# Kernel optimization log

Measured on AMD Instinct MI355X. Metric: run time of the kernel, lower is better.

The kernel has to match this reference:

```python
import jax, jax.numpy as jnp
import numpy as np


def position_encoding(feature_size, d_model):
    pos = jnp.arange(feature_size, dtype=jnp.float32)[:, None]
    _2i = jnp.arange(0, d_model, 2, dtype=jnp.float32)
    ang = pos / jnp.power(10000.0, _2i / d_model)  # [F, D/2]
    pe = jnp.zeros((feature_size, d_model), dtype=jnp.float32)
    pe = pe.at[:, 0::2].set(jnp.sin(ang))
    pe = pe.at[:, 1::2].set(jnp.cos(ang))
    return pe


def setup_inputs() -> dict:
    key = jax.random.key(0)
    ks = jax.random.split(key, 11)
    B, F, D, T, V = 32, 512, 256, 32, 128
    sc = 0.02
    return {
        "f": jax.random.normal(ks[0], (B, F, D), dtype=jnp.float32),
        "decoder_input_ids": jax.random.randint(ks[1], (B, T), 0, V),
        "emb": sc * jax.random.normal(ks[2], (V, D), dtype=jnp.float32),
        "w_e": sc * jax.random.normal(ks[3], (D, D), dtype=jnp.float32),
        "w_h": sc * jax.random.normal(ks[4], (D, D), dtype=jnp.float32),
        "w_f": sc * jax.random.normal(ks[5], (D, D), dtype=jnp.float32),
        "w_q": sc * jax.random.normal(ks[6], (D, D), dtype=jnp.float32),
        "w_s": sc * jax.random.normal(ks[7], (D, D), dtype=jnp.float32),
        "w_g": sc * jax.random.normal(ks[8], (D, 2 * D), dtype=jnp.float32),
        "w_ih": sc * jax.random.normal(ks[9], (4 * D, 2 * D), dtype=jnp.float32),
        "w_hh": sc * jax.random.normal(ks[10], (4 * D, D), dtype=jnp.float32),
    }


def reference(f, decoder_input_ids, emb, w_e, w_h, w_f, w_q, w_s, w_g, w_ih, w_hh):
    B, F, D = f.shape
    q = position_encoding(F, D)                      # [F, D]
    dec = emb[decoder_input_ids]                     # [B, T, D]
    # loop-invariant attention terms, hoisted: w_f(f) + w_q(q)
    base = jnp.einsum('bfd,od->bfo', f, w_f) + (q @ w_q.T)[None]  # [B, F, D]
    fq = f + q[None]                                 # [B, F, D]

    def step(carry, x_t):
        h, cell, s, cp = carry
        # LSTMCell (bias=False), torch gate order i, f, g, o
        xin = jnp.concatenate([x_t, cp], axis=-1)    # [B, 2D]
        gates = xin @ w_ih.T + h @ w_hh.T            # [B, 4D]
        gi, gf, gg, go = jnp.split(gates, 4, axis=-1)
        cell = jax.nn.sigmoid(gf) * cell + jax.nn.sigmoid(gi) * jnp.tanh(gg)
        h = jax.nn.sigmoid(go) * jnp.tanh(cell)
        # Bahdanau-style energy; softmax over feature (last) dim per source
        t_in = jnp.tanh((h @ w_h.T)[:, None] + base + jnp.einsum('bfd,od->bfo', s, w_s))
        e = jnp.einsum('bfd,od->bfo', t_in, w_e)     # [B, F, D]
        alpha = jax.nn.softmax(e, axis=-1)
        s = s + alpha
        c = (alpha * f).sum(1)                       # [B, D]
        cp = (alpha * fq).sum(1)                     # [B, D]
        pred = jnp.concatenate([c, h], axis=-1) @ w_g.T  # [B, D]
        return (h, cell, s, cp), pred

    z = jnp.zeros((B, D), dtype=f.dtype)
    carry0 = (z, z, jnp.zeros_like(f), z)
    _, preds = jax.lax.scan(step, carry0, jnp.swapaxes(dec, 0, 1))  # [T, B, D]
    return jnp.swapaxes(preds, 0, 1)                 # [B, T, D]
```

## Files before the change

kernel.cpp:

```cpp
#include <hip/hip_runtime.h>
#include <math.h>

#define NB 32
#define NF 512
#define ND 256
#define NT 32
#define RPB 32
#define NTILE (NF / RPB)

typedef __attribute__((ext_vector_type(8))) short bf16x8;
typedef __attribute__((ext_vector_type(4))) float f32x4;

__device__ __forceinline__ float sigmoidf_(float x) { return 1.0f / (1.0f + __expf(-x)); }

__device__ __forceinline__ short f2bf(float x) {
    union { float f; unsigned u; } v; v.f = x;
    unsigned r = (v.u + 0x7FFF + ((v.u >> 16) & 1)) >> 16;
    return (short)r;
}

__global__ void pe_kernel(float* __restrict__ q) {
    int p = blockIdx.x;
    int d = threadIdx.x;
    float i2 = (float)((d >> 1) << 1);
    float rate = expf(-9.210340371976184f * (i2 / (float)ND));
    float ang = (float)p * rate;
    q[p * ND + d] = (d & 1) ? cosf(ang) : sinf(ang);
}

__global__ void gather_kernel(const int* __restrict__ ids, const float* __restrict__ emb,
                              float* __restrict__ dec) {
    int bt = blockIdx.x;
    int d = threadIdx.x;
    dec[(size_t)bt * ND + d] = emb[(size_t)ids[bt] * ND + d];
}

__global__ void wcvt_kernel(const float* __restrict__ w, short* __restrict__ wb, int n) {
    int i = blockIdx.x * 256 + threadIdx.x;
    if (i < n) wb[i] = f2bf(w[i]);
}

__global__ void qwq_kernel(const float* __restrict__ q, const float* __restrict__ w_q,
                           float* __restrict__ qwq) {
    int p = blockIdx.x;
    int o = threadIdx.x;
    __shared__ float qs[ND];
    qs[o] = q[(size_t)p * ND + o];
    __syncthreads();
    const float4* wr = (const float4*)(w_q + (size_t)o * ND);
    float acc = 0.f;
    for (int k4 = 0; k4 < ND / 4; ++k4) {
        float4 w = wr[k4];
        int k = 4 * k4;
        acc += qs[k] * w.x + qs[k + 1] * w.y + qs[k + 2] * w.z + qs[k + 3] * w.w;
    }
    qwq[(size_t)p * ND + o] = acc;
}

__global__ void base_kernel(const float* __restrict__ fin, const float* __restrict__ w_f,
                            const float* __restrict__ qwq, float* __restrict__ bsum) {
    int b = blockIdx.x / NTILE;
    int f0 = (blockIdx.x % NTILE) * RPB;
    int o = threadIdx.x;
    __shared__ float fs[RPB][ND];
    #pragma unroll
    for (int r = 0; r < RPB; ++r)
        fs[r][o] = fin[((size_t)(b * NF + f0 + r)) * ND + o];
    __syncthreads();
    float acc[RPB];
    #pragma unroll
    for (int r = 0; r < RPB; ++r) acc[r] = 0.f;
    const float4* wr = (const float4*)(w_f + (size_t)o * ND);
    for (int k4 = 0; k4 < ND / 4; ++k4) {
        float4 w = wr[k4];
        int k = 4 * k4;
        #pragma unroll
        for (int r = 0; r < RPB; ++r)
            acc[r] += fs[r][k] * w.x + fs[r][k + 1] * w.y + fs[r][k + 2] * w.z + fs[r][k + 3] * w.w;
    }
    #pragma unroll
    for (int r = 0; r < RPB; ++r)
        bsum[((size_t)(b * NF + f0 + r)) * ND + o] = acc[r] + qwq[(size_t)(f0 + r) * ND + o];
}

#define ZSTRIDE 769
#define ZPSTRIDE 513
__global__ void gates_kernel(int t, int mode,
                             const float* __restrict__ dec,
                             const float* __restrict__ cpart, const float* __restrict__ cppart,
                             const float* __restrict__ h,
                             const float* __restrict__ w_ih, const float* __restrict__ w_hh,
                             const float* __restrict__ w_g,
                             float* __restrict__ gatesT, float* __restrict__ out) {
    extern __shared__ float lds[];
    int bid = blockIdx.x;
    int tid = threadIdx.x;

    if (bid < 128) {
        if (!(mode & 1)) return;
        int j0 = bid * 8;
        float* wl = lds;
        float* zl = lds + 8 * 768;
        float4* wl4 = (float4*)wl;
        for (int cc = 0; cc < 6; ++cc) {
            int idx4 = tid + cc * 256;
            int flat = idx4 * 4;
            int r = flat / 768;
            int col = flat - r * 768;
            float4 v;
            if (col < 512) v = *(const float4*)(w_ih + (size_t)(j0 + r) * 512 + col);
            else           v = *(const float4*)(w_hh + (size_t)(j0 + r) * 256 + (col - 512));
            wl4[idx4] = v;
        }
        for (int b = 0; b < NB; ++b) {
            int d = tid;
            float xv = (t < NT) ? dec[((size_t)b * NT + t) * ND + d] : 0.f;
            float cpsum = 0.f;
            if (t > 0) {
                #pragma unroll
                for (int tl = 0; tl < NTILE; ++tl)
                    cpsum += cppart[((size_t)tl * NB + b) * ND + d];
            }
            float hv = h[(size_t)b * ND + d];
            zl[b * ZSTRIDE + d]       = xv;
            zl[b * ZSTRIDE + 256 + d] = cpsum;
            zl[b * ZSTRIDE + 512 + d] = hv;
        }
        __syncthreads();
        int r = tid >> 5;
        int b = tid & 31;
        const float4* wr4 = (const float4*)(wl + r * 768);
        const float* zb = zl + b * ZSTRIDE;
        float acc = 0.f;
        #pragma unroll 8
        for (int k4 = 0; k4 < 192; ++k4) {
            float4 w = wr4[k4];
            int k = 4 * k4;
            acc += w.x * zb[k] + w.y * zb[k + 1] + w.z * zb[k + 2] + w.w * zb[k + 3];
        }
        gatesT[(size_t)(j0 + r) * NB + b] = acc;
    } else {
        if (!(mode & 2)) return;
        int p0 = (bid - 128) * 8;
        float* wl = lds;
        float* zl = lds + 8 * 512;
        float4* wl4 = (float4*)wl;
        for (int cc = 0; cc < 4; ++cc) {
            int idx4 = tid + cc * 256;
            int flat = idx4 * 4;
            int r = flat >> 9;
            int col = flat & 511;
            wl4[idx4] = *(const float4*)(w_g + (size_t)(p0 + r) * 512 + col);
        }
        for (int b = 0; b < NB; ++b) {
            float csum = 0.f;
            #pragma unroll
            for (int tl = 0; tl < NTILE; ++tl)
                csum += cpart[((size_t)tl * NB + b) * ND + tid];
            zl[b * ZPSTRIDE + tid]       = csum;
            zl[b * ZPSTRIDE + 256 + tid] = h[(size_t)b * ND + tid];
        }
        __syncthreads();
        int r = tid >> 5;
        int b = tid & 31;
        const float4* wr4 = (const float4*)(wl + r * 512);
        const float* zb = zl + b * ZPSTRIDE;
        float acc = 0.f;
        #pragma unroll 8
        for (int k4 = 0; k4 < 128; ++k4) {
            float4 w = wr4[k4];
            int k = 4 * k4;
            acc += w.x * zb[k] + w.y * zb[k + 1] + w.z * zb[k + 2] + w.w * zb[k + 3];
        }
        out[((size_t)b * NT + (t - 1)) * ND + p0 + r] = acc;
    }
}

__global__ void cell_hwh_kernel(const float* __restrict__ gatesT,
                                float* __restrict__ h, float* __restrict__ cell,
                                const float* __restrict__ w_h, float* __restrict__ hwh) {
    int b = blockIdx.x;
    int o = threadIdx.x;
    __shared__ float hn[ND];
    float gi = gatesT[(size_t)(0 * ND + o) * NB + b];
    float gf = gatesT[(size_t)(1 * ND + o) * NB + b];
    float gg = gatesT[(size_t)(2 * ND + o) * NB + b];
    float go = gatesT[(size_t)(3 * ND + o) * NB + b];
    float cold = cell[(size_t)b * ND + o];
    float cnew = sigmoidf_(gf) * cold + sigmoidf_(gi) * tanhf(gg);
    float hval = sigmoidf_(go) * tanhf(cnew);
    cell[(size_t)b * ND + o] = cnew;
    h[(size_t)b * ND + o] = hval;
    hn[o] = hval;
    __syncthreads();
    const float4* whr = (const float4*)(w_h + (size_t)o * ND);
    float a = 0.f;
    for (int k4 = 0; k4 < ND / 4; ++k4) {
        float4 w = whr[k4]; int k = 4 * k4;
        a += hn[k] * w.x + hn[k + 1] * w.y + hn[k + 2] * w.z + hn[k + 3] * w.w;
    }
    hwh[(size_t)b * ND + o] = a;
}

__global__ void attn_step_kernel(float* __restrict__ bsum,
                                 const float* __restrict__ fin, const float* __restrict__ q,
                                 const float* __restrict__ hwh,
                                 const short* __restrict__ w_e_bf, const short* __restrict__ w_s_bf,
                                 float* __restrict__ cpart, float* __restrict__ cppart) {
    int b = blockIdx.x / NTILE;
    int tile = blockIdx.x % NTILE;
    int f0 = tile * RPB;
    int tid = threadIdx.x;
    int l = tid & 63;
    int wv = tid >> 6;

    __shared__ __align__(16) short tin_bf[RPB * ND];
    __shared__ float sred[RPB][5];

    int o0 = wv * 64;
    int c15 = l & 15;
    int g = l >> 4;
    int kgrp = g * 8;
    char* tb = (char*)tin_bf;

    float bsv[2][4][4];
    {
        float hv4[4];
        #pragma unroll
        for (int nt = 0; nt < 4; ++nt)
            hv4[nt] = hwh[(size_t)b * ND + o0 + nt * 16 + c15];
        #pragma unroll
        for (int mt = 0; mt < 2; ++mt)
            #pragma unroll
            for (int reg = 0; reg < 4; ++reg) {
                int r = mt * 16 + g * 4 + reg;
                size_t rowb = ((size_t)(b * NF + f0 + r)) * ND;
                #pragma unroll
                for (int nt = 0; nt < 4; ++nt) {
                    int col = o0 + nt * 16 + c15;
                    float bs = bsum[rowb + col];
                    bsv[mt][nt][reg] = bs;
                    float tv = tanhf(hv4[nt] + bs);
                    int byte = (r * 512 + col * 2) ^ ((r & 7) << 4);
                    *(short*)(tb + byte) = f2bf(tv);
                }
            }
    }
    __syncthreads();

    f32x4 acc[2][4];
    #pragma unroll
    for (int mt = 0; mt < 2; ++mt)
        #pragma unroll
        for (int nt = 0; nt < 4; ++nt)
            acc[mt][nt] = (f32x4)0.f;
    #pragma unroll
    for (int ks = 0; ks < 8; ++ks) {
        int kb = ks * 32 + kgrp;
        bf16x8 afr[2];
        #pragma unroll
        for (int mt = 0; mt < 2; ++mt) {
            int row = mt * 16 + c15;
            int byte = (row * 512 + kb * 2) ^ ((row & 7) << 4);
            afr[mt] = *(const bf16x8*)(tb + byte);
        }
        #pragma unroll
        for (int nt = 0; nt < 4; ++nt) {
            int o = o0 + nt * 16 + c15;
            bf16x8 bfr = *(const bf16x8*)(w_e_bf + (size_t)o * ND + kb);
            #pragma unroll
            for (int mt = 0; mt < 2; ++mt)
                acc[mt][nt] = __builtin_amdgcn_mfma_f32_16x16x32_bf16(afr[mt], bfr, acc[mt][nt], 0, 0, 0);
        }
    }

    float ps[2][4];
    #pragma unroll
    for (int mt = 0; mt < 2; ++mt)
        #pragma unroll
        for (int reg = 0; reg < 4; ++reg) ps[mt][reg] = 0.f;
    #pragma unroll
    for (int mt = 0; mt < 2; ++mt)
        #pragma unroll
        for (int nt = 0; nt < 4; ++nt)
            #pragma unroll
            for (int reg = 0; reg < 4; ++reg) {
                float a = __expf(acc[mt][nt][reg]);
                acc[mt][nt][reg] = a;
                ps[mt][reg] += a;
            }
    #pragma unroll
    for (int off = 1; off <= 8; off <<= 1)
        #pragma unroll
        for (int mt = 0; mt < 2; ++mt)
            #pragma unroll
            for (int reg = 0; reg < 4; ++reg)
                ps[mt][reg] += __shfl_xor(ps[mt][reg], off);
    if (c15 == 0) {
        #pragma unroll
        for (int mt = 0; mt < 2; ++mt)
            #pragma unroll
            for (int reg = 0; reg < 4; ++reg)
                sred[mt * 16 + g * 4 + reg][wv] = ps[mt][reg];
    }
    __syncthreads();
    float inv[2][4];
    #pragma unroll
    for (int mt = 0; mt < 2; ++mt)
        #pragma unroll
        for (int reg = 0; reg < 4; ++reg) {
            int r = mt * 16 + g * 4 + reg;
            inv[mt][reg] = 1.0f / (sred[r][0] + sred[r][1] + sred[r][2] + sred[r][3]);
        }
    #pragma unroll
    for (int mt = 0; mt < 2; ++mt)
        #pragma unroll
        for (int nt = 0; nt < 4; ++nt)
            #pragma unroll
            for (int reg = 0; reg < 4; ++reg)
                acc[mt][nt][reg] *= inv[mt][reg];

    {
        float pc[4], pcp[4];
        #pragma unroll
        for (int nt = 0; nt < 4; ++nt) { pc[nt] = 0.f; pcp[nt] = 0.f; }
        #pragma unroll
        for (int mt = 0; mt < 2; ++mt)
            #pragma unroll
            for (int reg = 0; reg < 4; ++reg) {
                int r = mt * 16 + g * 4 + reg;
                size_t rowb = ((size_t)(b * NF + f0 + r)) * ND;
                size_t qrowb = (size_t)(f0 + r) * ND;
                #pragma unroll
                for (int nt = 0; nt < 4; ++nt) {
                    int col = o0 + nt * 16 + c15;
                    float a = acc[mt][nt][reg];
                    float fv = fin[rowb + col];
                    float qv = q[qrowb + col];
                    pc[nt] += a * fv;
                    pcp[nt] += a * (fv + qv);
                }
            }
        #pragma unroll
        for (int off = 16; off <= 32; off <<= 1)
            #pragma unroll
            for (int nt = 0; nt < 4; ++nt) {
                pc[nt]  += __shfl_xor(pc[nt], off);
                pcp[nt] += __shfl_xor(pcp[nt], off);
            }
        if (g == 0) {
            #pragma unroll
            for (int nt = 0; nt < 4; ++nt) {
                int col = o0 + nt * 16 + c15;
                cpart [((size_t)tile * NB + b) * ND + col] = pc[nt];
                cppart[((size_t)tile * NB + b) * ND + col] = pcp[nt];
            }
        }
    }

    #pragma unroll
    for (int mt = 0; mt < 2; ++mt)
        #pragma unroll
        for (int reg = 0; reg < 4; ++reg) {
            int r = mt * 16 + g * 4 + reg;
            #pragma unroll
            for (int nt = 0; nt < 4; ++nt) {
                int col = o0 + nt * 16 + c15;
                int byte = (r * 512 + col * 2) ^ ((r & 7) << 4);
                *(short*)(tb + byte) = f2bf(acc[mt][nt][reg]);
            }
        }
    __syncthreads();

    {
        f32x4 acc2[2][4];
        #pragma unroll
        for (int mt = 0; mt < 2; ++mt)
            #pragma unroll
            for (int nt = 0; nt < 4; ++nt)
                acc2[mt][nt] = (f32x4)0.f;
        #pragma unroll
        for (int ks = 0; ks < 8; ++ks) {
            int kb = ks * 32 + kgrp;
            bf16x8 afr[2];
            #pragma unroll
            for (int mt = 0; mt < 2; ++mt) {
                int row = mt * 16 + c15;
                int byte = (row * 512 + kb * 2) ^ ((row & 7) << 4);
                afr[mt] = *(const bf16x8*)(tb + byte);
            }
            #pragma unroll
            for (int nt = 0; nt < 4; ++nt) {
                int o = o0 + nt * 16 + c15;
                bf16x8 bfr = *(const bf16x8*)(w_s_bf + (size_t)o * ND + kb);
                #pragma unroll
                for (int mt = 0; mt < 2; ++mt)
                    acc2[mt][nt] = __builtin_amdgcn_mfma_f32_16x16x32_bf16(afr[mt], bfr, acc2[mt][nt], 0, 0, 0);
            }
        }
        #pragma unroll
        for (int mt = 0; mt < 2; ++mt)
            #pragma unroll
            for (int reg = 0; reg < 4; ++reg) {
                int r = mt * 16 + g * 4 + reg;
                size_t rowb = ((size_t)(b * NF + f0 + r)) * ND;
                #pragma unroll
                for (int nt = 0; nt < 4; ++nt) {
                    int col = o0 + nt * 16 + c15;
                    bsum[rowb + col] = bsv[mt][nt][reg] + acc2[mt][nt][reg];
                }
            }
    }
}

extern "C" void kernel_launch(void* const* d_in, const int* in_sizes, int n_in,
                              void* d_out, int out_size, void* d_ws, size_t ws_size,
                              hipStream_t stream) {
    const float* fin  = (const float*)d_in[0];
    const int*   ids  = (const int*)  d_in[1];
    const float* emb  = (const float*)d_in[2];
    const float* w_e  = (const float*)d_in[3];
    const float* w_h  = (const float*)d_in[4];
    const float* w_f  = (const float*)d_in[5];
    const float* w_q  = (const float*)d_in[6];
    const float* w_s  = (const float*)d_in[7];
    const float* w_g  = (const float*)d_in[8];
    const float* w_ih = (const float*)d_in[9];
    const float* w_hh = (const float*)d_in[10];
    float* out = (float*)d_out;
    float* ws  = (float*)d_ws;

    size_t off = 0;
    float* q      = ws + off; off += (size_t)NF * ND;
    float* scratch= ws + off; off += (size_t)NF * ND;
    float* dec    = ws + off; off += (size_t)NB * NT * ND;
    float* bsum   = ws + off; off += (size_t)NB * NF * ND;
    float* h      = ws + off; off += (size_t)NB * ND;
    float* cell   = ws + off; off += (size_t)NB * ND;
    float* hwh    = ws + off; off += (size_t)NB * ND;
    float* cpart  = ws + off; off += (size_t)NTILE * NB * ND;
    float* cppart = ws + off; off += (size_t)NTILE * NB * ND;
    short* w_e_bf = (short*)(ws + off); off += (size_t)ND * ND / 2;
    short* w_s_bf = (short*)(ws + off); off += (size_t)ND * ND / 2;

    float* qwq    = scratch;
    float* gatesT = scratch + 65536;

    hipMemsetAsync(h, 0, sizeof(float) * NB * ND, stream);
    hipMemsetAsync(cell, 0, sizeof(float) * NB * ND, stream);

    pe_kernel<<<NF, ND, 0, stream>>>(q);
    gather_kernel<<<NB * NT, ND, 0, stream>>>(ids, emb, dec);
    wcvt_kernel<<<ND * ND / 256, 256, 0, stream>>>(w_e, w_e_bf, ND * ND);
    wcvt_kernel<<<ND * ND / 256, 256, 0, stream>>>(w_s, w_s_bf, ND * ND);
    qwq_kernel<<<NF, ND, 0, stream>>>(q, w_q, qwq);
    base_kernel<<<NB * NTILE, ND, 0, stream>>>(fin, w_f, qwq, bsum);

    const size_t gates_lds = (size_t)(8 * 768 + NB * ZSTRIDE) * sizeof(float);

    for (int t = 0; t < NT; ++t) {
        int mode = (t > 0) ? 3 : 1;
        gates_kernel<<<160, ND, gates_lds, stream>>>(t, mode, dec, cpart, cppart, h,
                                                     w_ih, w_hh, w_g, gatesT, out);
        cell_hwh_kernel<<<NB, ND, 0, stream>>>(gatesT, h, cell, w_h, hwh);
        attn_step_kernel<<<NB * NTILE, ND, 0, stream>>>(bsum, fin, q, hwh,
                                                        w_e_bf, w_s_bf, cpart, cppart);
    }
    gates_kernel<<<160, ND, gates_lds, stream>>>(NT, 2, dec, cpart, cppart, h,
                                                 w_ih, w_hh, w_g, gatesT, out);
}
```

Before: 3.050 ms.

## Fuse LSTM cell and h·w_h into attention step kernel with double-buffered state

Removes the separate cell_hwh kernel. Every attention block now recomputes the LSTM cell update and the h·w_h matvec for its batch row; tile 0 writes the new h and cell into ping-pong buffers so no block overwrites state that another block is still reading. The gates layout is changed to batch-major so the fused reads are contiguous. The bsum, fin and q accesses are reworked through an LDS transpose buffer so each thread handles one column across rows, giving coalesced global loads and stores. This drops one launch and one global round trip per timestep. The cost is the matvec being repeated 16-fold per batch row, with strided w_h row reads from L2.

```diff
diff --git a/kernel.cpp b/kernel.cpp
--- a/kernel.cpp
+++ b/kernel.cpp
@@ -138,7 +138,7 @@
             int k = 4 * k4;
             acc += w.x * zb[k] + w.y * zb[k + 1] + w.z * zb[k + 2] + w.w * zb[k + 3];
         }
-        gatesT[(size_t)(j0 + r) * NB + b] = acc;
+        gatesT[(size_t)b * 1024 + (j0 + r)] = acc;
     } else {
         if (!(mode & 2)) return;
         int p0 = (bid - 128) * 8;
@@ -176,37 +176,15 @@
     }
 }
 
-__global__ void cell_hwh_kernel(const float* __restrict__ gatesT,
-                                float* __restrict__ h, float* __restrict__ cell,
-                                const float* __restrict__ w_h, float* __restrict__ hwh) {
-    int b = blockIdx.x;
-    int o = threadIdx.x;
-    __shared__ float hn[ND];
-    float gi = gatesT[(size_t)(0 * ND + o) * NB + b];
-    float gf = gatesT[(size_t)(1 * ND + o) * NB + b];
-    float gg = gatesT[(size_t)(2 * ND + o) * NB + b];
-    float go = gatesT[(size_t)(3 * ND + o) * NB + b];
-    float cold = cell[(size_t)b * ND + o];
-    float cnew = sigmoidf_(gf) * cold + sigmoidf_(gi) * tanhf(gg);
-    float hval = sigmoidf_(go) * tanhf(cnew);
-    cell[(size_t)b * ND + o] = cnew;
-    h[(size_t)b * ND + o] = hval;
-    hn[o] = hval;
-    __syncthreads();
-    const float4* whr = (const float4*)(w_h + (size_t)o * ND);
-    float a = 0.f;
-    for (int k4 = 0; k4 < ND / 4; ++k4) {
-        float4 w = whr[k4]; int k = 4 * k4;
-        a += hn[k] * w.x + hn[k + 1] * w.y + hn[k + 2] * w.z + hn[k + 3] * w.w;
-    }
-    hwh[(size_t)b * ND + o] = a;
-}
-
-__global__ void attn_step_kernel(float* __restrict__ bsum,
-                                 const float* __restrict__ fin, const float* __restrict__ q,
-                                 const float* __restrict__ hwh,
-                                 const short* __restrict__ w_e_bf, const short* __restrict__ w_s_bf,
-                                 float* __restrict__ cpart, float* __restrict__ cppart) {
+__global__ void __launch_bounds__(256) attn_step_kernel(
+        float* __restrict__ bsum,
+        const float* __restrict__ fin, const float* __restrict__ q,
+        const float* __restrict__ gatesT,
+        const float* __restrict__ cell_prev, float* __restrict__ cell_next,
+        float* __restrict__ h_next,
+        const float* __restrict__ w_h,
+        const short* __restrict__ w_e_bf, const short* __restrict__ w_s_bf,
+        float* __restrict__ cpart, float* __restrict__ cppart) {
     int b = blockIdx.x / NTILE;
     int tile = blockIdx.x % NTILE;
     int f0 = tile * RPB;
@@ -215,36 +193,47 @@
     int wv = tid >> 6;
 
     __shared__ __align__(16) short tin_bf[RPB * ND];
+    __shared__ float xfer[RPB * 257];
+    __shared__ float hn[ND];
     __shared__ float sred[RPB][5];
 
     int o0 = wv * 64;
     int c15 = l & 15;
     int g = l >> 4;
-    int kgrp = g * 8;
     char* tb = (char*)tin_bf;
 
-    float bsv[2][4][4];
     {
-        float hv4[4];
-        #pragma unroll
-        for (int nt = 0; nt < 4; ++nt)
-            hv4[nt] = hwh[(size_t)b * ND + o0 + nt * 16 + c15];
-        #pragma unroll
-        for (int mt = 0; mt < 2; ++mt)
-            #pragma unroll
-            for (int reg = 0; reg < 4; ++reg) {
-                int r = mt * 16 + g * 4 + reg;
-                size_t rowb = ((size_t)(b * NF + f0 + r)) * ND;
-                #pragma unroll
-                for (int nt = 0; nt < 4; ++nt) {
-                    int col = o0 + nt * 16 + c15;
-                    float bs = bsum[rowb + col];
-                    bsv[mt][nt][reg] = bs;
-                    float tv = tanhf(hv4[nt] + bs);
-                    int byte = (r * 512 + col * 2) ^ ((r & 7) << 4);
-                    *(short*)(tb + byte) = f2bf(tv);
-                }
-            }
+        float gi = gatesT[(size_t)b * 1024 + tid];
+        float gf = gatesT[(size_t)b * 1024 + 256 + tid];
+        float gg = gatesT[(size_t)b * 1024 + 512 + tid];
+        float go = gatesT[(size_t)b * 1024 + 768 + tid];
+        float cold = cell_prev[(size_t)b * ND + tid];
+        float cnew = sigmoidf_(gf) * cold + sigmoidf_(gi) * tanhf(gg);
+        float hval = sigmoidf_(go) * tanhf(cnew);
+        if (tile == 0) {
+            cell_next[(size_t)b * ND + tid] = cnew;
+            h_next[(size_t)b * ND + tid] = hval;
+        }
+        hn[tid] = hval;
+    }
+    __syncthreads();
+    float hwh_reg = 0.f;
+    {
+        const float4* whr = (const float4*)(w_h + (size_t)tid * ND);
+        #pragma unroll 8
+        for (int k4 = 0; k4 < ND / 4; ++k4) {
+            float4 w = whr[k4]; int k = 4 * k4;
+            hwh_reg += hn[k] * w.x + hn[k + 1] * w.y + hn[k + 2] * w.z + hn[k + 3] * w.w;
+        }
+    }
+
+    float bsv[RPB];
+    #pragma unroll
+    for (int r = 0; r < RPB; ++r) {
+        float bs = bsum[((size_t)(b * NF + f0 + r)) * ND + tid];
+        bsv[r] = bs;
+        int byte = (r * 512 + tid * 2) ^ ((r & 7) << 4);
+        *(short*)(tb + byte) = f2bf(tanhf(hwh_reg + bs));
     }
     __syncthreads();
 
@@ -256,7 +245,7 @@
             acc[mt][nt] = (f32x4)0.f;
     #pragma unroll
     for (int ks = 0; ks < 8; ++ks) {
-        int kb = ks * 32 + kgrp;
+        int kb = ks * 32 + g * 8;
         bf16x8 afr[2];
         #pragma unroll
         for (int mt = 0; mt < 2; ++mt) {
@@ -274,102 +263,75 @@
         }
     }
 
-    float ps[2][4];
-    #pragma unroll
-    for (int mt = 0; mt < 2; ++mt)
-        #pragma unroll
-        for (int reg = 0; reg < 4; ++reg) ps[mt][reg] = 0.f;
-    #pragma unroll
-    for (int mt = 0; mt < 2; ++mt)
-        #pragma unroll
-        for (int nt = 0; nt < 4; ++nt)
+    {
+        float ps[2][4];
+        #pragma unroll
+        for (int mt = 0; mt < 2; ++mt)
+            #pragma unroll
+            for (int reg = 0; reg < 4; ++reg) ps[mt][reg] = 0.f;
+        #pragma unroll
+        for (int mt = 0; mt < 2; ++mt)
+            #pragma unroll
+            for (int nt = 0; nt < 4; ++nt)
+                #pragma unroll
+                for (int reg = 0; reg < 4; ++reg) {
+                    float a = __expf(acc[mt][nt][reg]);
+                    acc[mt][nt][reg] = a;
+                    ps[mt][reg] += a;
+                }
+        #pragma unroll
+        for (int off = 1; off <= 8; off <<= 1)
+            #pragma unroll
+            for (int mt = 0; mt < 2; ++mt)
+                #pragma unroll
+                for (int reg = 0; reg < 4; ++reg)
+                    ps[mt][reg] += __shfl_xor(ps[mt][reg], off);
+        if (c15 == 0) {
+            #pragma unroll
+            for (int mt = 0; mt < 2; ++mt)
+                #pragma unroll
+                for (int reg = 0; reg < 4; ++reg)
+                    sred[mt * 16 + g * 4 + reg][wv] = ps[mt][reg];
+        }
+        __syncthreads();
+        #pragma unroll
+        for (int mt = 0; mt < 2; ++mt)
             #pragma unroll
             for (int reg = 0; reg < 4; ++reg) {
-                float a = __expf(acc[mt][nt][reg]);
-                acc[mt][nt][reg] = a;
-                ps[mt][reg] += a;
+                int r = mt * 16 + g * 4 + reg;
+                float inv = 1.0f / (sred[r][0] + sred[r][1] + sred[r][2] + sred[r][3]);
+                #pragma unroll
+                for (int nt = 0; nt < 4; ++nt)
+                    acc[mt][nt][reg] *= inv;
             }
-    #pragma unroll
-    for (int off = 1; off <= 8; off <<= 1)
-        #pragma unroll
-        for (int mt = 0; mt < 2; ++mt)
-            #pragma unroll
-            for (int reg = 0; reg < 4; ++reg)
-                ps[mt][reg] += __shfl_xor(ps[mt][reg], off);
-    if (c15 == 0) {
-        #pragma unroll
-        for (int mt = 0; mt < 2; ++mt)
-            #pragma unroll
-            for (int reg = 0; reg < 4; ++reg)
-                sred[mt * 16 + g * 4 + reg][wv] = ps[mt][reg];
-    }
-    __syncthreads();
-    float inv[2][4];
+    }
+
     #pragma unroll
     for (int mt = 0; mt < 2; ++mt)
         #pragma unroll
         for (int reg = 0; reg < 4; ++reg) {
             int r = mt * 16 + g * 4 + reg;
-            inv[mt][reg] = 1.0f / (sred[r][0] + sred[r][1] + sred[r][2] + sred[r][3]);
-        }
-    #pragma unroll
-    for (int mt = 0; mt < 2; ++mt)
-        #pragma unroll
-        for (int nt = 0; nt < 4; ++nt)
-            #pragma unroll
-            for (int reg = 0; reg < 4; ++reg)
-                acc[mt][nt][reg] *= inv[mt][reg];
+            #pragma unroll
+            for (int nt = 0; nt < 4; ++nt)
+                xfer[r * 257 + o0 + nt * 16 + c15] = acc[mt][nt][reg];
+        }
+    __syncthreads();
 
     {
-        float pc[4], pcp[4];
-        #pragma unroll
-        for (int nt = 0; nt < 4; ++nt) { pc[nt] = 0.f; pcp[nt] = 0.f; }
-        #pragma unroll
-        for (int mt = 0; mt < 2; ++mt)
-            #pragma unroll
-            for (int reg = 0; reg < 4; ++reg) {
-                int r = mt * 16 + g * 4 + reg;
-                size_t rowb = ((size_t)(b * NF + f0 + r)) * ND;
-                size_t qrowb = (size_t)(f0 + r) * ND;
-                #pragma unroll
-                for (int nt = 0; nt < 4; ++nt) {
-                    int col = o0 + nt * 16 + c15;
-                    float a = acc[mt][nt][reg];
-                    float fv = fin[rowb + col];
-                    float qv = q[qrowb + col];
-                    pc[nt] += a * fv;
-                    pcp[nt] += a * (fv + qv);
-                }
-            }
-        #pragma unroll
-        for (int off = 16; off <= 32; off <<= 1)
-            #pragma unroll
-            for (int nt = 0; nt < 4; ++nt) {
-                pc[nt]  += __shfl_xor(pc[nt], off);
-                pcp[nt] += __shfl_xor(pcp[nt], off);
-            }
-        if (g == 0) {
-            #pragma unroll
-            for (int nt = 0; nt < 4; ++nt) {
-                int col = o0 + nt * 16 + c15;
-                cpart [((size_t)tile * NB + b) * ND + col] = pc[nt];
-                cppart[((size_t)tile * NB + b) * ND + col] = pcp[nt];
-            }
-        }
-    }
-
-    #pragma unroll
-    for (int mt = 0; mt < 2; ++mt)
-        #pragma unroll
-        for (int reg = 0; reg < 4; ++reg) {
-            int r = mt * 16 + g * 4 + reg;
-            #pragma unroll
-            for (int nt = 0; nt < 4; ++nt) {
-                int col = o0 + nt * 16 + c15;
-                int byte = (r * 512 + col * 2) ^ ((r & 7) << 4);
-                *(short*)(tb + byte) = f2bf(acc[mt][nt][reg]);
-            }
-        }
+        float pc = 0.f, pcp = 0.f;
+        #pragma unroll
+        for (int r = 0; r < RPB; ++r) {
+            float a = xfer[r * 257 + tid];
+            float fv = fin[((size_t)(b * NF + f0 + r)) * ND + tid];
+            float qv = q[(size_t)(f0 + r) * ND + tid];
+            pc += a * fv;
+            pcp += a * (fv + qv);
+            int byte = (r * 512 + tid * 2) ^ ((r & 7) << 4);
+            *(short*)(tb + byte) = f2bf(a);
+        }
+        cpart [((size_t)tile * NB + b) * ND + tid] = pc;
+        cppart[((size_t)tile * NB + b) * ND + tid] = pcp;
+    }
     __syncthreads();
 
     {
@@ -381,7 +343,7 @@
                 acc2[mt][nt] = (f32x4)0.f;
         #pragma unroll
         for (int ks = 0; ks < 8; ++ks) {
-            int kb = ks * 32 + kgrp;
+            int kb = ks * 32 + g * 8;
             bf16x8 afr[2];
             #pragma unroll
             for (int mt = 0; mt < 2; ++mt) {
@@ -403,14 +365,16 @@
             #pragma unroll
             for (int reg = 0; reg < 4; ++reg) {
                 int r = mt * 16 + g * 4 + reg;
-                size_t rowb = ((size_t)(b * NF + f0 + r)) * ND;
-                #pragma unroll
-                for (int nt = 0; nt < 4; ++nt) {
-                    int col = o0 + nt * 16 + c15;
-                    bsum[rowb + col] = bsv[mt][nt][reg] + acc2[mt][nt][reg];
-                }
+                #pragma unroll
+                for (int nt = 0; nt < 4; ++nt)
+                    xfer[r * 257 + o0 + nt * 16 + c15] = acc2[mt][nt][reg];
             }
     }
+    __syncthreads();
+
+    #pragma unroll
+    for (int r = 0; r < RPB; ++r)
+        bsum[((size_t)(b * NF + f0 + r)) * ND + tid] = bsv[r] + xfer[r * 257 + tid];
 }
 
 extern "C" void kernel_launch(void* const* d_in, const int* in_sizes, int n_in,
@@ -435,19 +399,23 @@
     float* scratch= ws + off; off += (size_t)NF * ND;
     float* dec    = ws + off; off += (size_t)NB * NT * ND;
     float* bsum   = ws + off; off += (size_t)NB * NF * ND;
-    float* h      = ws + off; off += (size_t)NB * ND;
-    float* cell   = ws + off; off += (size_t)NB * ND;
-    float* hwh    = ws + off; off += (size_t)NB * ND;
+    float* h0     = ws + off; off += (size_t)NB * ND;
+    float* h1     = ws + off; off += (size_t)NB * ND;
+    float* cell0  = ws + off; off += (size_t)NB * ND;
+    float* cell1  = ws + off; off += (size_t)NB * ND;
     float* cpart  = ws + off; off += (size_t)NTILE * NB * ND;
     float* cppart = ws + off; off += (size_t)NTILE * NB * ND;
     short* w_e_bf = (short*)(ws + off); off += (size_t)ND * ND / 2;
     short* w_s_bf = (short*)(ws + off); off += (size_t)ND * ND / 2;
 
     float* qwq    = scratch;
-    float* gatesT = scratch + 65536;
-
-    hipMemsetAsync(h, 0, sizeof(float) * NB * ND, stream);
-    hipMemsetAsync(cell, 0, sizeof(float) * NB * ND, stream);
+    float* gatesT = scratch;
+
+    float* hbuf[2]    = { h0, h1 };
+    float* cellbuf[2] = { cell0, cell1 };
+
+    hipMemsetAsync(h0, 0, sizeof(float) * NB * ND, stream);
+    hipMemsetAsync(cell0, 0, sizeof(float) * NB * ND, stream);
 
     pe_kernel<<<NF, ND, 0, stream>>>(q);
     gather_kernel<<<NB * NT, ND, 0, stream>>>(ids, emb, dec);
@@ -460,12 +428,13 @@
 
     for (int t = 0; t < NT; ++t) {
         int mode = (t > 0) ? 3 : 1;
-        gates_kernel<<<160, ND, gates_lds, stream>>>(t, mode, dec, cpart, cppart, h,
+        int p = t & 1;
+        gates_kernel<<<160, ND, gates_lds, stream>>>(t, mode, dec, cpart, cppart, hbuf[p],
                                                      w_ih, w_hh, w_g, gatesT, out);
-        cell_hwh_kernel<<<NB, ND, 0, stream>>>(gatesT, h, cell, w_h, hwh);
-        attn_step_kernel<<<NB * NTILE, ND, 0, stream>>>(bsum, fin, q, hwh,
-                                                        w_e_bf, w_s_bf, cpart, cppart);
-    }
-    gates_kernel<<<160, ND, gates_lds, stream>>>(NT, 2, dec, cpart, cppart, h,
+        attn_step_kernel<<<NB * NTILE, ND, 0, stream>>>(bsum, fin, q, gatesT,
+                                                        cellbuf[p], cellbuf[p ^ 1], hbuf[p ^ 1],
+                                                        w_h, w_e_bf, w_s_bf, cpart, cppart);
+    }
+    gates_kernel<<<160, ND, gates_lds, stream>>>(NT, 2, dec, cpart, cppart, hbuf[0],
                                                  w_ih, w_hh, w_g, gatesT, out);
 }
```

After: 2.676 ms. 1.14x faster.
